# Optimization experiments

Measured on AMD Instinct MI355X. Metric: run time of the kernel, lower is better.

Reference implementation:

```python
import jax, jax.numpy as jnp
import numpy as np

B, S, T, D = 8, 8, 256, 256          # batch, series, time_steps, input_dim
H, DK = 8, 64                         # attn_heads, attn_dim
HD = H * DK                           # 512
L = 2                                 # attn_layers
F = 256                               # mlp_dim
R = 512                               # resolution
M = 128                               # number of mid-points sampled this step
EPS = 1e-5


def setup_inputs() -> dict:
    key = jax.random.key(0)
    ks = iter(jax.random.split(key, 64))

    def rn(shape, scale=0.05):
        return scale * jax.random.normal(next(ks), shape, dtype=jnp.float32)

    inp = {
        'encoded': jax.random.normal(next(ks), (B, S, T, D), dtype=jnp.float32),
        'true_u': jax.random.uniform(next(ks), (B, S, T), dtype=jnp.float32),
        'mid_idx': jnp.sort(jax.random.randint(next(ks), (M,), 0, T)),
        'left_idx': jax.random.randint(next(ks), (M,), 0, T),
        'right_idx': jax.random.randint(next(ks), (M,), 0, T),
        'i': 3,
        # dimension_shift
        'ds_W': rn((D, HD)), 'ds_b': jnp.zeros((HD,), jnp.float32),
        # per-layer, per-head key-creator MLPs (stacked): (D+1) -> F -> F -> DK
        'kW1': rn((L, H, D + 1, F)), 'kb1': jnp.zeros((L, H, F), jnp.float32),
        'kW2': rn((L, H, F, F)),     'kb2': jnp.zeros((L, H, F), jnp.float32),
        'kW3': rn((L, H, F, DK)),    'kb3': jnp.zeros((L, H, DK), jnp.float32),
        # value-creator MLPs
        'vW1': rn((L, H, D + 1, F)), 'vb1': jnp.zeros((L, H, F), jnp.float32),
        'vW2': rn((L, H, F, F)),     'vb2': jnp.zeros((L, H, F), jnp.float32),
        'vW3': rn((L, H, F, DK)),    'vb3': jnp.zeros((L, H, DK), jnp.float32),
        # attention / feed-forward layer norms
        'ln1_g': jnp.ones((L, HD), jnp.float32), 'ln1_b': jnp.zeros((L, HD), jnp.float32),
        'ln2_g': jnp.ones((L, HD), jnp.float32), 'ln2_b': jnp.zeros((L, HD), jnp.float32),
        # feed-forwards
        'ffW1': rn((L, HD, HD)), 'ffb1': jnp.zeros((L, HD), jnp.float32),
        'ffW2': rn((L, HD, HD)), 'ffb2': jnp.zeros((L, HD), jnp.float32),
        # dist_extractors MLP: HD -> F -> F -> R
        'deW1': rn((HD, F)), 'deb1': jnp.zeros((F,), jnp.float32),
        'deW2': rn((F, F)),  'deb2': jnp.zeros((F,), jnp.float32),
        'deW3': rn((F, R)),  'deb3': jnp.zeros((R,), jnp.float32),
    }
    return inp


def _mlp_heads(x, W1, b1, W2, b2, W3, b3):
    # x: [B,S,T,D+1]; weights: [L,H,...] -> out [L,B,S,T,H,DK]
    h = jax.nn.relu(jnp.einsum('bstc,lhcf->lbsthf', x, W1) + b1[:, None, None, None])
    h = jax.nn.relu(jnp.einsum('lbsthf,lhfg->lbsthg', h, W2) + b2[:, None, None, None])
    return jnp.einsum('lbsthg,lhgd->lbsthd', h, W3) + b3[:, None, None, None]


def _ln(x, g, b):
    mu = jnp.mean(x, axis=-1, keepdims=True)
    var = jnp.mean(jnp.square(x - mu), axis=-1, keepdims=True)
    return (x - mu) * jax.lax.rsqrt(var + EPS) * g + b


def reference(encoded, true_u, mid_idx, left_idx, right_idx, i,
              ds_W, ds_b,
              kW1, kb1, kW2, kb2, kW3, kb3,
              vW1, vb1, vW2, vb2, vW3, vb3,
              ln1_g, ln1_b, ln2_g, ln2_b,
              ffW1, ffb1, ffW2, ffb2,
              deW1, deb1, deW2, deb2, deW3, deb3):
    # merged_input = cat([encoded, true_u[..., None]])  -> [B,S,T,D+1]
    merged = jnp.concatenate([encoded, true_u[..., None]], axis=-1)

    keys = _mlp_heads(merged, kW1, kb1, kW2, kb2, kW3, kb3)   # [L,B,S,T,H,DK]
    values = _mlp_heads(merged, vW1, vb1, vW2, vb2, vW3, vb3)  # [L,B,S,T,H,DK]

    srange = jnp.arange(S)
    # n=1 neighbor: time index = loop counter m for series < i, else right[m]
    # (faithful to keys_hist[:, :i, mid:mid+1] in the original)
    idx1 = jnp.where(srange[None, :] < i, jnp.arange(M)[:, None], right_idx[:, None])  # [M,S]

    def gather_neighbors(kv):  # kv: [L,B,S,T,H,DK] -> [L,B,M,S,2,H,DK]
        n0 = jnp.transpose(kv[:, :, :, left_idx], (0, 1, 3, 2, 4, 5))  # [L,B,M,S,H,DK]
        n1 = kv[:, :, srange[None, :], idx1]                            # [L,B,M,S,H,DK]
        return jnp.stack([n0, n1], axis=4)

    nk = gather_neighbors(keys)
    nv = gather_neighbors(values)

    pred = encoded[:, i, mid_idx]                  # [B,M,D]
    att_value = pred @ ds_W + ds_b                 # [B,M,HD]

    scale = DK ** (-0.5)
    for l in range(L):
        avh = att_value.reshape(B, M, H, DK)
        prod = jnp.einsum('bmhd,bmsnhd->bmhsn', avh, nk[l]) * scale
        w = jax.nn.softmax(prod, axis=-1)          # softmax over n only, as in source
        att = jnp.einsum('bmhsn,bmsnhd->bmhd', w, nv[l]).reshape(B, M, HD)
        x = _ln(att_value + att, ln1_g[l], ln1_b[l])
        ff = jax.nn.relu(x @ ffW1[l] + ffb1[l]) @ ffW2[l] + ffb2[l]
        att_value = _ln(x + ff, ln2_g[l], ln2_b[l])

    h = jax.nn.relu(att_value @ deW1 + deb1)
    h = jax.nn.relu(h @ deW2 + deb2)
    logits = h @ deW3 + deb3                       # [B,M,R]
    return logits
```

## Files before the change

kernel.cpp:

```cpp
#include <hip/hip_runtime.h>
#include <hip/hip_bf16.h>

#define NB 8
#define NS 8
#define NT 256
#define ND 256
#define NH 8
#define NDK 64
#define NHD 512
#define NL 2
#define NF 256
#define NR 512
#define NM 128
#define NTOK 16384
#define NROW 1024

typedef __attribute__((ext_vector_type(8))) short short8;
typedef __attribute__((ext_vector_type(4))) float f32x4;

__device__ __forceinline__ unsigned short f2bf(float x) {
    unsigned u = __builtin_bit_cast(unsigned, x);
    unsigned r = (u + 0x7fffu + ((u >> 16) & 1u)) >> 16;
    return (unsigned short)r;
}
__device__ __forceinline__ float bf2f(unsigned short x) {
    return __builtin_bit_cast(float, ((unsigned)x) << 16);
}
__device__ __forceinline__ float wred(float v) {
#pragma unroll
    for (int o = 32; o > 0; o >>= 1) v += __shfl_xor(v, o, 64);
    return v;
}

__global__ __launch_bounds__(256) void prep_all(
    const float* __restrict__ enc,
    const float* __restrict__ kW1, const float* __restrict__ kW2, const float* __restrict__ kW3,
    const float* __restrict__ vW1, const float* __restrict__ vW2, const float* __restrict__ vW3,
    const float* __restrict__ dsW, const float* __restrict__ ffW1,
    const float* __restrict__ ffW2, const float* __restrict__ deW1,
    const float* __restrict__ deW2, const float* __restrict__ deW3,
    unsigned short* __restrict__ XF, unsigned short* __restrict__ WP,
    float* __restrict__ W1L, unsigned short* __restrict__ WG) {
    __shared__ float T[32][257];
    int bid = blockIdx.x, tid = threadIdx.x;
    if (bid < 512) {
        int t0 = bid * 32;
        const float* src = enc + (size_t)t0 * 256;
#pragma unroll
        for (int it = 0; it < 8; ++it) {
            int f4 = it * 256 + tid;
            int row = f4 >> 6, c = (f4 & 63) * 4;
            float4 v = *(const float4*)(src + row * 256 + c);
            T[row][c] = v.x; T[row][c + 1] = v.y; T[row][c + 2] = v.z; T[row][c + 3] = v.w;
        }
        __syncthreads();
        int tile = t0 >> 7, g = (t0 >> 6) & 1, nt0 = (t0 >> 4) & 3;
#pragma unroll
        for (int i = 0; i < 32; i += 8) {
            int o = tid * 32 + i;
            int lane = (o >> 3) & 63, ntp = (o >> 9) & 1, kc = o >> 10;
            int id = lane & 15, quad = lane >> 4;
            __align__(16) unsigned short p[8];
#pragma unroll
            for (int j = 0; j < 8; ++j) p[j] = f2bf(T[ntp * 16 + id][kc * 32 + quad * 8 + j]);
            size_t dsto = ((size_t)((((tile * 8 + kc) * 2 + g) * 4 + (nt0 + ntp)) * 64 + lane)) * 8;
            *(uint4*)(XF + dsto) = *(uint4*)p;
        }
    } else if (bid < 1280) {
        int lb = bid - 512;
        int combo = lb / 24, r = lb % 24;
        int st = r >> 3, kc = r & 7;
        int kvv = combo >> 4, l = (combo >> 3) & 1, h = combo & 7;
        unsigned short* dstc = WP + (size_t)combo * 147456;
        if (st < 2) {
            const float* W = (st == 0) ? (kvv ? vW1 : kW1) : (kvv ? vW2 : kW2);
            int rows = (st == 0) ? 257 : 256;
            const float* src = W + ((size_t)(l * 8 + h) * rows + kc * 32) * 256;
#pragma unroll
            for (int it = 0; it < 8; ++it) {
                int f4 = it * 256 + tid;
                int row = f4 >> 6, c = (f4 & 63) * 4;
                float4 v = *(const float4*)(src + (size_t)row * 256 + c);
                T[row][c] = v.x; T[row][c + 1] = v.y; T[row][c + 2] = v.z; T[row][c + 3] = v.w;
            }
            __syncthreads();
            unsigned short* dst = dstc + st * 65536 + kc * 8192;
#pragma unroll
            for (int i = 0; i < 32; i += 8) {
                int o = tid * 32 + i;
                int lane = (o >> 3) & 63, ftile = o >> 9;
                int id = lane & 15, quad = lane >> 4;
                __align__(16) unsigned short p[8];
#pragma unroll
                for (int j = 0; j < 8; ++j) p[j] = f2bf(T[quad * 8 + j][ftile * 16 + id]);
                *(uint4*)(dst + o) = *(uint4*)p;
            }
            if (st == 0 && kc == 0) {
                const float* hw = (kvv ? vW1 : kW1) + (size_t)(l * 8 + h) * 257 * 256;
                W1L[combo * 256 + tid] = hw[65536 + tid];
            }
        } else {
            const float* src = (kvv ? vW3 : kW3) + ((size_t)(l * 8 + h) * 256 + kc * 32) * 64;
#pragma unroll
            for (int it = 0; it < 2; ++it) {
                int f4 = it * 256 + tid;
                int row = f4 >> 4, c = (f4 & 15) * 4;
                float4 v = *(const float4*)(src + (size_t)row * 64 + c);
                T[row][c] = v.x; T[row][c + 1] = v.y; T[row][c + 2] = v.z; T[row][c + 3] = v.w;
            }
            __syncthreads();
            unsigned short* dst = dstc + 131072 + kc * 2048;
            int o = tid * 8;
            int lane = tid & 63, ftile = tid >> 6;
            int id = lane & 15, quad = lane >> 4;
            __align__(16) unsigned short p[8];
#pragma unroll
            for (int j = 0; j < 8; ++j) p[j] = f2bf(T[quad * 8 + j][ftile * 16 + id]);
            *(uint4*)(dst + o) = *(uint4*)p;
        }
    } else {
        int lb0 = bid - 1280;
        const float* src; int N, kc, ng; size_t base;
        if (lb0 < 32)       { int lb = lb0;       src = dsW;           N = 512; base = 0;       kc = lb >> 2; ng = lb & 3; }
        else if (lb0 < 96)  { int lb = lb0 - 32;  src = ffW1;          N = 512; base = 131072;  kc = lb >> 2; ng = lb & 3; }
        else if (lb0 < 160) { int lb = lb0 - 96;  src = ffW1 + 262144; N = 512; base = 393216;  kc = lb >> 2; ng = lb & 3; }
        else if (lb0 < 224) { int lb = lb0 - 160; src = ffW2;          N = 512; base = 655360;  kc = lb >> 2; ng = lb & 3; }
        else if (lb0 < 288) { int lb = lb0 - 224; src = ffW2 + 262144; N = 512; base = 917504;  kc = lb >> 2; ng = lb & 3; }
        else if (lb0 < 320) { int lb = lb0 - 288; src = deW1;          N = 256; base = 1179648; kc = lb >> 1; ng = lb & 1; }
        else if (lb0 < 336) { int lb = lb0 - 320; src = deW2;          N = 256; base = 1310720; kc = lb >> 1; ng = lb & 1; }
        else                { int lb = lb0 - 336; src = deW3;          N = 512; base = 1376256; kc = lb >> 2; ng = lb & 3; }
        int NTl = N >> 4;
        const float* s = src + (size_t)(kc * 32) * N + ng * 128;
#pragma unroll
        for (int it = 0; it < 4; ++it) {
            int f4 = it * 256 + tid;
            int row = f4 >> 5, c = (f4 & 31) * 4;
            float4 v = *(const float4*)(s + (size_t)row * N + c);
            T[row][c] = v.x; T[row][c + 1] = v.y; T[row][c + 2] = v.z; T[row][c + 3] = v.w;
        }
        __syncthreads();
        unsigned short* d = WG + base + (size_t)(kc * NTl + ng * 8) * 512;
#pragma unroll
        for (int i = 0; i < 16; i += 8) {
            int o = tid * 16 + i;
            int lane = (o >> 3) & 63, ntl = o >> 9;
            int id = lane & 15, quad = lane >> 4;
            __align__(16) unsigned short p[8];
#pragma unroll
            for (int j = 0; j < 8; ++j) p[j] = f2bf(T[quad * 8 + j][ntl * 16 + id]);
            *(uint4*)(d + o) = *(uint4*)p;
        }
    }
}

__global__ __launch_bounds__(256, 4) void heads_mlp(
    const float* __restrict__ tu, const unsigned short* __restrict__ XF,
    const unsigned short* __restrict__ WP, const float* __restrict__ W1L,
    const float* __restrict__ kb1, const float* __restrict__ kb2, const float* __restrict__ kb3,
    const float* __restrict__ vb1, const float* __restrict__ vb2, const float* __restrict__ vb3,
    unsigned short* __restrict__ KV) {
    __shared__ __align__(16) unsigned short smem[16896];

    const int tid = threadIdx.x;
    const int w2 = tid >> 6, lane = tid & 63, id = lane & 15, quad = lane >> 4;
    const int combo = blockIdx.x & 31, t64 = blockIdx.x >> 5;
    const int kvv = combo >> 4, l = (combo >> 3) & 1, h = combo & 7;
    const int r0 = t64 * 64;
    const int tile128 = t64 >> 1, g = t64 & 1;
    const unsigned short* WF1 = WP + (size_t)combo * 147456;
    const unsigned short* WF2 = WF1 + 65536;
    const unsigned short* WF3 = WF1 + 131072;
    const float* b1 = (kvv ? vb1 : kb1) + (l * 8 + h) * 256;
    const float* b2 = (kvv ? vb2 : kb2) + (l * 8 + h) * 256;
    const float* b3 = (kvv ? vb3 : kb3) + (l * 8 + h) * 64;

    {
        const uint4* s = (const uint4*)(XF + (size_t)tile128 * 32768 + g * 2048);
        uint4* d = (uint4*)smem;
#pragma unroll
        for (int kc = 0; kc < 8; ++kc) d[kc * 256 + tid] = s[kc * 512 + tid];
    }
    __syncthreads();

    f32x4 acc[4][4];
#pragma unroll
    for (int i = 0; i < 4; ++i)
#pragma unroll
        for (int j = 0; j < 4; ++j) acc[i][j] = (f32x4){0.f, 0.f, 0.f, 0.f};

    {
        short8 af[4], afn[4];
#pragma unroll
        for (int ft = 0; ft < 4; ++ft)
            af[ft] = *(const short8*)(WF1 + (size_t)((w2 * 4 + ft) * 64 + lane) * 8);
#pragma unroll
        for (int kc = 0; kc < 8; ++kc) {
            if (kc < 7) {
#pragma unroll
                for (int ft = 0; ft < 4; ++ft)
                    afn[ft] = *(const short8*)(WF1 + (size_t)(((kc + 1) * 16 + w2 * 4 + ft) * 64 + lane) * 8);
            }
            short8 bf[4];
#pragma unroll
            for (int nt = 0; nt < 4; ++nt)
                bf[nt] = *(const short8*)(smem + (size_t)(kc * 4 + nt) * 512 + lane * 8);
#pragma unroll
            for (int ft = 0; ft < 4; ++ft)
#pragma unroll
                for (int nt = 0; nt < 4; ++nt)
                    acc[ft][nt] = __builtin_amdgcn_mfma_f32_16x16x32_bf16(af[ft], bf[nt], acc[ft][nt], 0, 0, 0);
#pragma unroll
            for (int ft = 0; ft < 4; ++ft) af[ft] = afn[ft];
        }
    }
    __syncthreads();
    {
        float ur[4];
#pragma unroll
        for (int nt = 0; nt < 4; ++nt) ur[nt] = tu[r0 + nt * 16 + id];
#pragma unroll
        for (int ft = 0; ft < 4; ++ft) {
            int fb = w2 * 64 + ft * 16 + quad * 4;
            float4 bb = *(const float4*)(b1 + fb);
            float4 wl = *(const float4*)(W1L + combo * 256 + fb);
            const float* bbp = (const float*)&bb;
            const float* wlp = (const float*)&wl;
#pragma unroll
            for (int nt = 0; nt < 4; ++nt) {
                unsigned short p[4];
#pragma unroll
                for (int r = 0; r < 4; ++r) {
                    float v = acc[ft][nt][r] + bbp[r] + ur[nt] * wlp[r];
                    p[r] = f2bf(fmaxf(v, 0.f));
                }
                uint2 pk;
                pk.x = (unsigned)p[0] | ((unsigned)p[1] << 16);
                pk.y = (unsigned)p[2] | ((unsigned)p[3] << 16);
                *(uint2*)(smem + (size_t)(nt * 16 + id) * 264 + fb) = pk;
            }
        }
    }
    __syncthreads();

#pragma unroll
    for (int i = 0; i < 4; ++i)
#pragma unroll
        for (int j = 0; j < 4; ++j) acc[i][j] = (f32x4){0.f, 0.f, 0.f, 0.f};
    {
        short8 af[4], afn[4];
#pragma unroll
        for (int ft = 0; ft < 4; ++ft)
            af[ft] = *(const short8*)(WF2 + (size_t)((w2 * 4 + ft) * 64 + lane) * 8);
#pragma unroll
        for (int kc = 0; kc < 8; ++kc) {
            if (kc < 7) {
#pragma unroll
                for (int ft = 0; ft < 4; ++ft)
                    afn[ft] = *(const short8*)(WF2 + (size_t)(((kc + 1) * 16 + w2 * 4 + ft) * 64 + lane) * 8);
            }
            short8 bf[4];
#pragma unroll
            for (int nt = 0; nt < 4; ++nt)
                bf[nt] = *(const short8*)(smem + (size_t)(nt * 16 + id) * 264 + kc * 32 + quad * 8);
#pragma unroll
            for (int ft = 0; ft < 4; ++ft)
#pragma unroll
                for (int nt = 0; nt < 4; ++nt)
                    acc[ft][nt] = __builtin_amdgcn_mfma_f32_16x16x32_bf16(af[ft], bf[nt], acc[ft][nt], 0, 0, 0);
#pragma unroll
            for (int ft = 0; ft < 4; ++ft) af[ft] = afn[ft];
        }
    }
    __syncthreads();
#pragma unroll
    for (int ft = 0; ft < 4; ++ft) {
        int fb = w2 * 64 + ft * 16 + quad * 4;
        float4 bb = *(const float4*)(b2 + fb);
        const float* bbp = (const float*)&bb;
#pragma unroll
        for (int nt = 0; nt < 4; ++nt) {
            unsigned short p[4];
#pragma unroll
            for (int r = 0; r < 4; ++r)
                p[r] = f2bf(fmaxf(acc[ft][nt][r] + bbp[r], 0.f));
            uint2 pk;
            pk.x = (unsigned)p[0] | ((unsigned)p[1] << 16);
            pk.y = (unsigned)p[2] | ((unsigned)p[3] << 16);
            *(uint2*)(smem + (size_t)(nt * 16 + id) * 264 + fb) = pk;
        }
    }
    __syncthreads();

    f32x4 a3[4];
#pragma unroll
    for (int i = 0; i < 4; ++i) a3[i] = (f32x4){0.f, 0.f, 0.f, 0.f};
    {
        short8 af3[4], af3n[4];
#pragma unroll
        for (int ft = 0; ft < 4; ++ft)
            af3[ft] = *(const short8*)(WF3 + (size_t)(ft * 64 + lane) * 8);
#pragma unroll
        for (int kc = 0; kc < 8; ++kc) {
            if (kc < 7) {
#pragma unroll
                for (int ft = 0; ft < 4; ++ft)
                    af3n[ft] = *(const short8*)(WF3 + (size_t)(((kc + 1) * 4 + ft) * 64 + lane) * 8);
            }
            short8 b3f = *(const short8*)(smem + (size_t)(w2 * 16 + id) * 264 + kc * 32 + quad * 8);
#pragma unroll
            for (int ft = 0; ft < 4; ++ft)
                a3[ft] = __builtin_amdgcn_mfma_f32_16x16x32_bf16(af3[ft], b3f, a3[ft], 0, 0, 0);
#pragma unroll
            for (int ft = 0; ft < 4; ++ft) af3[ft] = af3n[ft];
        }
    }
    __syncthreads();
    {
        int tl = w2 * 16 + id;
#pragma unroll
        for (int ft = 0; ft < 4; ++ft) {
            int dk0 = ft * 16 + quad * 4;
            float4 bb = *(const float4*)(b3 + dk0);
            const float* bbp = (const float*)&bb;
            unsigned short p[4];
#pragma unroll
            for (int r = 0; r < 4; ++r) p[r] = f2bf(a3[ft][r] + bbp[r]);
            uint2 pk;
            pk.x = (unsigned)p[0] | ((unsigned)p[1] << 16);
            pk.y = (unsigned)p[2] | ((unsigned)p[3] << 16);
            *(uint2*)(smem + (size_t)tl * 72 + dk0) = pk;
        }
    }
    __syncthreads();
    {
#pragma unroll
        for (int it = 0; it < 2; ++it) {
            int tl = it * 32 + (tid >> 3), part = tid & 7;
            uint4 v = *(const uint4*)(smem + (size_t)tl * 72 + part * 8);
            size_t base = ((size_t)((l * 2 + kvv) * NTOK + r0 + tl)) * 512 + h * 64 + part * 8;
            *(uint4*)(KV + base) = v;
        }
    }
}

__global__ __launch_bounds__(256) void gemm_ds(
    const float* __restrict__ enc, const int* __restrict__ mid,
    const int* __restrict__ ip, const unsigned short* __restrict__ WF,
    const float* __restrict__ bias, float* __restrict__ outf) {
    int tid = threadIdx.x, wv = tid >> 6, lane = tid & 63;
    int id = lane & 15, quad = lane >> 4;
    int ntile = blockIdx.x * 4 + wv;
    int n0 = ntile * 16, m0 = blockIdx.y * 32;
    int iv = ip[0];
    int r0 = m0 + id, r1 = m0 + 16 + id;
    const float* a0p = enc + (((size_t)((r0 >> 7) * 8 + iv)) * 256 + mid[r0 & 127]) * 256 + quad * 8;
    const float* a1p = enc + (((size_t)((r1 >> 7) * 8 + iv)) * 256 + mid[r1 & 127]) * 256 + quad * 8;
    f32x4 acc[2];
    acc[0] = (f32x4){0.f, 0.f, 0.f, 0.f};
    acc[1] = (f32x4){0.f, 0.f, 0.f, 0.f};
#pragma unroll
    for (int kc = 0; kc < 8; ++kc) {
        short8 bw = *(const short8*)(WF + (size_t)((kc * 32 + ntile) * 64 + lane) * 8);
        float4 u0 = *(const float4*)(a0p + kc * 32);
        float4 u1 = *(const float4*)(a0p + kc * 32 + 4);
        float4 w0 = *(const float4*)(a1p + kc * 32);
        float4 w1 = *(const float4*)(a1p + kc * 32 + 4);
        short8 a0, a1;
        a0[0] = (short)f2bf(u0.x); a0[1] = (short)f2bf(u0.y); a0[2] = (short)f2bf(u0.z); a0[3] = (short)f2bf(u0.w);
        a0[4] = (short)f2bf(u1.x); a0[5] = (short)f2bf(u1.y); a0[6] = (short)f2bf(u1.z); a0[7] = (short)f2bf(u1.w);
        a1[0] = (short)f2bf(w0.x); a1[1] = (short)f2bf(w0.y); a1[2] = (short)f2bf(w0.z); a1[3] = (short)f2bf(w0.w);
        a1[4] = (short)f2bf(w1.x); a1[5] = (short)f2bf(w1.y); a1[6] = (short)f2bf(w1.z); a1[7] = (short)f2bf(w1.w);
        acc[0] = __builtin_amdgcn_mfma_f32_16x16x32_bf16(a0, bw, acc[0], 0, 0, 0);
        acc[1] = __builtin_amdgcn_mfma_f32_16x16x32_bf16(a1, bw, acc[1], 0, 0, 0);
    }
    float bv = bias[n0 + id];
#pragma unroll
    for (int mt = 0; mt < 2; ++mt) {
#pragma unroll
        for (int r = 0; r < 4; ++r) {
            int row = m0 + mt * 16 + quad * 4 + r;
            outf[(size_t)row * 512 + n0 + id] = acc[mt][r] + bv;
        }
    }
}

__global__ __launch_bounds__(256) void gemm_bf16(
    const unsigned short* __restrict__ A, const unsigned short* __restrict__ WF,
    const float* __restrict__ bias, const float* __restrict__ res,
    float* __restrict__ outf, unsigned short* __restrict__ outb,
    int K, int N, int relu) {
    int tid = threadIdx.x, wv = tid >> 6, lane = tid & 63;
    int id = lane & 15, quad = lane >> 4;
    int ntile = blockIdx.x * 4 + wv;
    int n0 = ntile * 16, m0 = blockIdx.y * 32;
    int NTl = N >> 4, KC = K >> 5;
    f32x4 acc[2];
    acc[0] = (f32x4){0.f, 0.f, 0.f, 0.f};
    acc[1] = (f32x4){0.f, 0.f, 0.f, 0.f};
    short8 bw = *(const short8*)(WF + (size_t)(ntile * 64 + lane) * 8);
    short8 a0 = *(const short8*)(A + (size_t)(m0 + id) * K + quad * 8);
    short8 a1 = *(const short8*)(A + (size_t)(m0 + 16 + id) * K + quad * 8);
    for (int kc = 0; kc < KC; ++kc) {
        short8 bwn, a0n, a1n;
        if (kc + 1 < KC) {
            bwn = *(const short8*)(WF + (size_t)(((kc + 1) * NTl + ntile) * 64 + lane) * 8);
            a0n = *(const short8*)(A + (size_t)(m0 + id) * K + (kc + 1) * 32 + quad * 8);
            a1n = *(const short8*)(A + (size_t)(m0 + 16 + id) * K + (kc + 1) * 32 + quad * 8);
        }
        acc[0] = __builtin_amdgcn_mfma_f32_16x16x32_bf16(a0, bw, acc[0], 0, 0, 0);
        acc[1] = __builtin_amdgcn_mfma_f32_16x16x32_bf16(a1, bw, acc[1], 0, 0, 0);
        bw = bwn; a0 = a0n; a1 = a1n;
    }
    float bv = bias[n0 + id];
#pragma unroll
    for (int mt = 0; mt < 2; ++mt) {
#pragma unroll
        for (int r = 0; r < 4; ++r) {
            int row = m0 + mt * 16 + quad * 4 + r;
            int n = n0 + id;
            float v = acc[mt][r] + bv;
            if (res) v += res[(size_t)row * N + n];
            if (relu) v = fmaxf(v, 0.f);
            if (outf) outf[(size_t)row * N + n] = v;
            if (outb) outb[(size_t)row * N + n] = f2bf(v);
        }
    }
}

__global__ __launch_bounds__(256) void attn_ln(
    const float* __restrict__ attv, const unsigned short* __restrict__ keys,
    const unsigned short* __restrict__ vals, const int* __restrict__ left,
    const int* __restrict__ right, const int* __restrict__ ip,
    const float* __restrict__ g, const float* __restrict__ bb,
    float* __restrict__ xout, unsigned short* __restrict__ xoutb) {
    int tid = threadIdx.x, wv = tid >> 6, lane = tid & 63;
    int gid = blockIdx.x * 4 + wv;
    int b = gid >> 7, m = gid & 127;
    int iv = ip[0];
    int lt = left[m], rt = right[m];
    float av8[8], att8[8];
    {
        const float* avp = attv + (size_t)gid * 512 + lane * 8;
        float4 u0 = *(const float4*)(avp);
        float4 u1 = *(const float4*)(avp + 4);
        av8[0] = u0.x; av8[1] = u0.y; av8[2] = u0.z; av8[3] = u0.w;
        av8[4] = u1.x; av8[5] = u1.y; av8[6] = u1.z; av8[7] = u1.w;
    }
#pragma unroll
    for (int j = 0; j < 8; ++j) att8[j] = 0.f;
    for (int s = 0; s < 8; ++s) {
        int t1 = (s < iv) ? m : rt;
        size_t row0 = ((size_t)((b * 8 + s) * 256 + lt)) * 512 + lane * 8;
        size_t row1 = ((size_t)((b * 8 + s) * 256 + t1)) * 512 + lane * 8;
        uint4 k0u = *(const uint4*)(keys + row0);
        uint4 k1u = *(const uint4*)(keys + row1);
        uint4 v0u = *(const uint4*)(vals + row0);
        uint4 v1u = *(const uint4*)(vals + row1);
        const unsigned short* k0 = (const unsigned short*)&k0u;
        const unsigned short* k1 = (const unsigned short*)&k1u;
        const unsigned short* v0 = (const unsigned short*)&v0u;
        const unsigned short* v1 = (const unsigned short*)&v1u;
        float p0 = 0.f, p1 = 0.f;
#pragma unroll
        for (int j = 0; j < 8; ++j) {
            p0 += av8[j] * bf2f(k0[j]);
            p1 += av8[j] * bf2f(k1[j]);
        }
#pragma unroll
        for (int o = 1; o < 8; o <<= 1) {
            p0 += __shfl_xor(p0, o, 64);
            p1 += __shfl_xor(p1, o, 64);
        }
        p0 *= 0.125f; p1 *= 0.125f;
        float mx = fmaxf(p0, p1);
        float e0 = __expf(p0 - mx), e1 = __expf(p1 - mx);
        float inv = 1.f / (e0 + e1);
        float w0 = e0 * inv, w1 = e1 * inv;
#pragma unroll
        for (int j = 0; j < 8; ++j)
            att8[j] += w0 * bf2f(v0[j]) + w1 * bf2f(v1[j]);
    }
    float x8[8], sum = 0.f;
#pragma unroll
    for (int j = 0; j < 8; ++j) { x8[j] = av8[j] + att8[j]; sum += x8[j]; }
    float mu = wred(sum) * (1.f / 512.f);
    float s2 = 0.f;
#pragma unroll
    for (int j = 0; j < 8; ++j) { float d = x8[j] - mu; s2 += d * d; }
    float rs = rsqrtf(wred(s2) * (1.f / 512.f) + 1e-5f);
    {
        const float* gp = g + lane * 8;
        const float* bp = bb + lane * 8;
        float* of = xout + (size_t)gid * 512 + lane * 8;
        unsigned short* ob = xoutb + (size_t)gid * 512 + lane * 8;
        __align__(16) float vout[8];
        __align__(16) unsigned short pb[8];
#pragma unroll
        for (int j = 0; j < 8; ++j) {
            float v = (x8[j] - mu) * rs * gp[j] + bp[j];
            vout[j] = v; pb[j] = f2bf(v);
        }
        *(float4*)(of) = *(float4*)vout;
        *(float4*)(of + 4) = *(float4*)(vout + 4);
        *(uint4*)(ob) = *(uint4*)pb;
    }
}

__global__ __launch_bounds__(256) void ln_k(const float* __restrict__ in,
                                            const float* __restrict__ g,
                                            const float* __restrict__ bb,
                                            float* __restrict__ out,
                                            unsigned short* __restrict__ outb) {
    int tid = threadIdx.x, wv = tid >> 6, lane = tid & 63;
    int gid = blockIdx.x * 4 + wv;
    float x8[8], sum = 0.f;
    {
        const float* ip = in + (size_t)gid * 512 + lane * 8;
        float4 u0 = *(const float4*)(ip);
        float4 u1 = *(const float4*)(ip + 4);
        x8[0] = u0.x; x8[1] = u0.y; x8[2] = u0.z; x8[3] = u0.w;
        x8[4] = u1.x; x8[5] = u1.y; x8[6] = u1.z; x8[7] = u1.w;
    }
#pragma unroll
    for (int j = 0; j < 8; ++j) sum += x8[j];
    float mu = wred(sum) * (1.f / 512.f);
    float s2 = 0.f;
#pragma unroll
    for (int j = 0; j < 8; ++j) { float d = x8[j] - mu; s2 += d * d; }
    float rs = rsqrtf(wred(s2) * (1.f / 512.f) + 1e-5f);
    {
        const float* gp = g + lane * 8;
        const float* bp = bb + lane * 8;
        float* of = out + (size_t)gid * 512 + lane * 8;
        unsigned short* ob = outb + (size_t)gid * 512 + lane * 8;
        __align__(16) float vout[8];
        __align__(16) unsigned short pb[8];
#pragma unroll
        for (int j = 0; j < 8; ++j) {
            float v = (x8[j] - mu) * rs * gp[j] + bp[j];
            vout[j] = v; pb[j] = f2bf(v);
        }
        *(float4*)(of) = *(float4*)vout;
        *(float4*)(of + 4) = *(float4*)(vout + 4);
        *(uint4*)(ob) = *(uint4*)pb;
    }
}

extern "C" void kernel_launch(void* const* d_in, const int* in_sizes, int n_in,
                              void* d_out, int out_size, void* d_ws, size_t ws_size,
                              hipStream_t stream) {
    const float* encoded = (const float*)d_in[0];
    const float* true_u  = (const float*)d_in[1];
    const int* mid_idx   = (const int*)d_in[2];
    const int* left_idx  = (const int*)d_in[3];
    const int* right_idx = (const int*)d_in[4];
    const int* ip        = (const int*)d_in[5];
    const float* ds_W = (const float*)d_in[6];
    const float* ds_b = (const float*)d_in[7];
    const float* kW1 = (const float*)d_in[8];
    const float* kb1 = (const float*)d_in[9];
    const float* kW2 = (const float*)d_in[10];
    const float* kb2 = (const float*)d_in[11];
    const float* kW3 = (const float*)d_in[12];
    const float* kb3 = (const float*)d_in[13];
    const float* vW1 = (const float*)d_in[14];
    const float* vb1 = (const float*)d_in[15];
    const float* vW2 = (const float*)d_in[16];
    const float* vb2 = (const float*)d_in[17];
    const float* vW3 = (const float*)d_in[18];
    const float* vb3 = (const float*)d_in[19];
    const float* ln1_g = (const float*)d_in[20];
    const float* ln1_b = (const float*)d_in[21];
    const float* ln2_g = (const float*)d_in[22];
    const float* ln2_b = (const float*)d_in[23];
    const float* ffW1 = (const float*)d_in[24];
    const float* ffb1 = (const float*)d_in[25];
    const float* ffW2 = (const float*)d_in[26];
    const float* ffb2 = (const float*)d_in[27];
    const float* deW1 = (const float*)d_in[28];
    const float* deb1 = (const float*)d_in[29];
    const float* deW2 = (const float*)d_in[30];
    const float* deb2 = (const float*)d_in[31];
    const float* deW3 = (const float*)d_in[32];
    const float* deb3 = (const float*)d_in[33];

    char* ws = (char*)d_ws;
    unsigned short* XF   = (unsigned short*)(ws + 0);
    unsigned short* WP   = (unsigned short*)(ws + 8388608);
    float* W1L           = (float*)(ws + 17825792);
    unsigned short* KV   = (unsigned short*)(ws + 17858560);
    unsigned short* WG   = (unsigned short*)(ws + 84967424);
    float* ATTV          = (float*)(ws + 87982080);
    float* XBUF          = (float*)(ws + 90079232);
    float* YBUF          = (float*)(ws + 92176384);
    unsigned short* ATTVB = (unsigned short*)(ws + 94797824);
    unsigned short* XBUFB = (unsigned short*)(ws + 95846400);
    unsigned short* FBUFB = (unsigned short*)(ws + 96894976);
    unsigned short* DE1B = XBUFB;
    unsigned short* DE2B = FBUFB;

    unsigned short* WGds  = WG + 0;
    unsigned short* WGff1_0 = WG + 131072;
    unsigned short* WGff1_1 = WG + 393216;
    unsigned short* WGff2_0 = WG + 655360;
    unsigned short* WGff2_1 = WG + 917504;
    unsigned short* WGde1 = WG + 1179648;
    unsigned short* WGde2 = WG + 1310720;
    unsigned short* WGde3 = WG + 1376256;

    prep_all<<<1648, 256, 0, stream>>>(encoded, kW1, kW2, kW3, vW1, vW2, vW3,
                                       ds_W, ffW1, ffW2, deW1, deW2, deW3,
                                       XF, WP, W1L, WG);
    heads_mlp<<<8192, 256, 0, stream>>>(true_u, XF, WP, W1L, kb1, kb2, kb3,
                                        vb1, vb2, vb3, KV);
    gemm_ds<<<dim3(8, 32), 256, 0, stream>>>(encoded, mid_idx, ip, WGds, ds_b, ATTV);
    for (int l = 0; l < 2; ++l) {
        const unsigned short* keys = KV + (size_t)(l * 2) * NTOK * NHD;
        const unsigned short* vals = KV + (size_t)(l * 2 + 1) * NTOK * NHD;
        attn_ln<<<256, 256, 0, stream>>>(ATTV, keys, vals, left_idx, right_idx, ip,
                                         ln1_g + l * 512, ln1_b + l * 512, XBUF, XBUFB);
        gemm_bf16<<<dim3(8, 32), 256, 0, stream>>>(XBUFB, (l ? WGff1_1 : WGff1_0),
                                                   ffb1 + l * 512, nullptr,
                                                   nullptr, FBUFB, 512, 512, 1);
        gemm_bf16<<<dim3(8, 32), 256, 0, stream>>>(FBUFB, (l ? WGff2_1 : WGff2_0),
                                                   ffb2 + l * 512, XBUF,
                                                   YBUF, nullptr, 512, 512, 0);
        ln_k<<<256, 256, 0, stream>>>(YBUF, ln2_g + l * 512, ln2_b + l * 512, ATTV, ATTVB);
    }
    gemm_bf16<<<dim3(4, 32), 256, 0, stream>>>(ATTVB, WGde1, deb1, nullptr,
                                               nullptr, DE1B, 512, 256, 1);
    gemm_bf16<<<dim3(4, 32), 256, 0, stream>>>(DE1B, WGde2, deb2, nullptr,
                                               nullptr, DE2B, 256, 256, 1);
    gemm_bf16<<<dim3(8, 32), 256, 0, stream>>>(DE2B, WGde3, deb3, nullptr,
                                               (float*)d_out, nullptr, 256, 512, 0);
}
```

Measured before the change: 431.0 us.

## Fuse attention, feed-forward, layer norms and decoder MLP into one tail kernel

```diff
diff --git a/kernel.cpp b/kernel.cpp
--- a/kernel.cpp
+++ b/kernel.cpp
@@ -163,7 +163,7 @@
 
     const int tid = threadIdx.x;
     const int w2 = tid >> 6, lane = tid & 63, id = lane & 15, quad = lane >> 4;
-    const int combo = blockIdx.x & 31, t64 = blockIdx.x >> 5;
+    const int combo = blockIdx.x >> 8, t64 = blockIdx.x & 255;
     const int kvv = combo >> 4, l = (combo >> 3) & 1, h = combo & 7;
     const int r0 = t64 * 64;
     const int tile128 = t64 >> 1, g = t64 & 1;
@@ -337,212 +337,328 @@
         for (int it = 0; it < 2; ++it) {
             int tl = it * 32 + (tid >> 3), part = tid & 7;
             uint4 v = *(const uint4*)(smem + (size_t)tl * 72 + part * 8);
-            size_t base = ((size_t)((l * 2 + kvv) * NTOK + r0 + tl)) * 512 + h * 64 + part * 8;
+            size_t base = ((size_t)combo << 20) + (size_t)(r0 + tl) * 64 + part * 8;
             *(uint4*)(KV + base) = v;
         }
     }
 }
 
-__global__ __launch_bounds__(256) void gemm_ds(
+__global__ __launch_bounds__(256) void fused_tail(
     const float* __restrict__ enc, const int* __restrict__ mid,
-    const int* __restrict__ ip, const unsigned short* __restrict__ WF,
-    const float* __restrict__ bias, float* __restrict__ outf) {
-    int tid = threadIdx.x, wv = tid >> 6, lane = tid & 63;
-    int id = lane & 15, quad = lane >> 4;
-    int ntile = blockIdx.x * 4 + wv;
-    int n0 = ntile * 16, m0 = blockIdx.y * 32;
-    int iv = ip[0];
-    int r0 = m0 + id, r1 = m0 + 16 + id;
-    const float* a0p = enc + (((size_t)((r0 >> 7) * 8 + iv)) * 256 + mid[r0 & 127]) * 256 + quad * 8;
-    const float* a1p = enc + (((size_t)((r1 >> 7) * 8 + iv)) * 256 + mid[r1 & 127]) * 256 + quad * 8;
-    f32x4 acc[2];
-    acc[0] = (f32x4){0.f, 0.f, 0.f, 0.f};
-    acc[1] = (f32x4){0.f, 0.f, 0.f, 0.f};
-#pragma unroll
-    for (int kc = 0; kc < 8; ++kc) {
-        short8 bw = *(const short8*)(WF + (size_t)((kc * 32 + ntile) * 64 + lane) * 8);
-        float4 u0 = *(const float4*)(a0p + kc * 32);
-        float4 u1 = *(const float4*)(a0p + kc * 32 + 4);
-        float4 w0 = *(const float4*)(a1p + kc * 32);
-        float4 w1 = *(const float4*)(a1p + kc * 32 + 4);
-        short8 a0, a1;
-        a0[0] = (short)f2bf(u0.x); a0[1] = (short)f2bf(u0.y); a0[2] = (short)f2bf(u0.z); a0[3] = (short)f2bf(u0.w);
-        a0[4] = (short)f2bf(u1.x); a0[5] = (short)f2bf(u1.y); a0[6] = (short)f2bf(u1.z); a0[7] = (short)f2bf(u1.w);
-        a1[0] = (short)f2bf(w0.x); a1[1] = (short)f2bf(w0.y); a1[2] = (short)f2bf(w0.z); a1[3] = (short)f2bf(w0.w);
-        a1[4] = (short)f2bf(w1.x); a1[5] = (short)f2bf(w1.y); a1[6] = (short)f2bf(w1.z); a1[7] = (short)f2bf(w1.w);
-        acc[0] = __builtin_amdgcn_mfma_f32_16x16x32_bf16(a0, bw, acc[0], 0, 0, 0);
-        acc[1] = __builtin_amdgcn_mfma_f32_16x16x32_bf16(a1, bw, acc[1], 0, 0, 0);
-    }
-    float bv = bias[n0 + id];
-#pragma unroll
-    for (int mt = 0; mt < 2; ++mt) {
-#pragma unroll
-        for (int r = 0; r < 4; ++r) {
-            int row = m0 + mt * 16 + quad * 4 + r;
-            outf[(size_t)row * 512 + n0 + id] = acc[mt][r] + bv;
-        }
-    }
-}
-
-__global__ __launch_bounds__(256) void gemm_bf16(
-    const unsigned short* __restrict__ A, const unsigned short* __restrict__ WF,
-    const float* __restrict__ bias, const float* __restrict__ res,
-    float* __restrict__ outf, unsigned short* __restrict__ outb,
-    int K, int N, int relu) {
-    int tid = threadIdx.x, wv = tid >> 6, lane = tid & 63;
-    int id = lane & 15, quad = lane >> 4;
-    int ntile = blockIdx.x * 4 + wv;
-    int n0 = ntile * 16, m0 = blockIdx.y * 32;
-    int NTl = N >> 4, KC = K >> 5;
-    f32x4 acc[2];
-    acc[0] = (f32x4){0.f, 0.f, 0.f, 0.f};
-    acc[1] = (f32x4){0.f, 0.f, 0.f, 0.f};
-    short8 bw = *(const short8*)(WF + (size_t)(ntile * 64 + lane) * 8);
-    short8 a0 = *(const short8*)(A + (size_t)(m0 + id) * K + quad * 8);
-    short8 a1 = *(const short8*)(A + (size_t)(m0 + 16 + id) * K + quad * 8);
-    for (int kc = 0; kc < KC; ++kc) {
-        short8 bwn, a0n, a1n;
-        if (kc + 1 < KC) {
-            bwn = *(const short8*)(WF + (size_t)(((kc + 1) * NTl + ntile) * 64 + lane) * 8);
-            a0n = *(const short8*)(A + (size_t)(m0 + id) * K + (kc + 1) * 32 + quad * 8);
-            a1n = *(const short8*)(A + (size_t)(m0 + 16 + id) * K + (kc + 1) * 32 + quad * 8);
-        }
-        acc[0] = __builtin_amdgcn_mfma_f32_16x16x32_bf16(a0, bw, acc[0], 0, 0, 0);
-        acc[1] = __builtin_amdgcn_mfma_f32_16x16x32_bf16(a1, bw, acc[1], 0, 0, 0);
-        bw = bwn; a0 = a0n; a1 = a1n;
-    }
-    float bv = bias[n0 + id];
-#pragma unroll
-    for (int mt = 0; mt < 2; ++mt) {
-#pragma unroll
-        for (int r = 0; r < 4; ++r) {
-            int row = m0 + mt * 16 + quad * 4 + r;
-            int n = n0 + id;
-            float v = acc[mt][r] + bv;
-            if (res) v += res[(size_t)row * N + n];
-            if (relu) v = fmaxf(v, 0.f);
-            if (outf) outf[(size_t)row * N + n] = v;
-            if (outb) outb[(size_t)row * N + n] = f2bf(v);
-        }
-    }
-}
-
-__global__ __launch_bounds__(256) void attn_ln(
-    const float* __restrict__ attv, const unsigned short* __restrict__ keys,
-    const unsigned short* __restrict__ vals, const int* __restrict__ left,
-    const int* __restrict__ right, const int* __restrict__ ip,
-    const float* __restrict__ g, const float* __restrict__ bb,
-    float* __restrict__ xout, unsigned short* __restrict__ xoutb) {
-    int tid = threadIdx.x, wv = tid >> 6, lane = tid & 63;
-    int gid = blockIdx.x * 4 + wv;
-    int b = gid >> 7, m = gid & 127;
-    int iv = ip[0];
-    int lt = left[m], rt = right[m];
-    float av8[8], att8[8];
-    {
-        const float* avp = attv + (size_t)gid * 512 + lane * 8;
-        float4 u0 = *(const float4*)(avp);
-        float4 u1 = *(const float4*)(avp + 4);
-        av8[0] = u0.x; av8[1] = u0.y; av8[2] = u0.z; av8[3] = u0.w;
-        av8[4] = u1.x; av8[5] = u1.y; av8[6] = u1.z; av8[7] = u1.w;
-    }
-#pragma unroll
-    for (int j = 0; j < 8; ++j) att8[j] = 0.f;
-    for (int s = 0; s < 8; ++s) {
-        int t1 = (s < iv) ? m : rt;
-        size_t row0 = ((size_t)((b * 8 + s) * 256 + lt)) * 512 + lane * 8;
-        size_t row1 = ((size_t)((b * 8 + s) * 256 + t1)) * 512 + lane * 8;
-        uint4 k0u = *(const uint4*)(keys + row0);
-        uint4 k1u = *(const uint4*)(keys + row1);
-        uint4 v0u = *(const uint4*)(vals + row0);
-        uint4 v1u = *(const uint4*)(vals + row1);
-        const unsigned short* k0 = (const unsigned short*)&k0u;
-        const unsigned short* k1 = (const unsigned short*)&k1u;
-        const unsigned short* v0 = (const unsigned short*)&v0u;
-        const unsigned short* v1 = (const unsigned short*)&v1u;
-        float p0 = 0.f, p1 = 0.f;
-#pragma unroll
-        for (int j = 0; j < 8; ++j) {
-            p0 += av8[j] * bf2f(k0[j]);
-            p1 += av8[j] * bf2f(k1[j]);
-        }
-#pragma unroll
-        for (int o = 1; o < 8; o <<= 1) {
-            p0 += __shfl_xor(p0, o, 64);
-            p1 += __shfl_xor(p1, o, 64);
-        }
-        p0 *= 0.125f; p1 *= 0.125f;
-        float mx = fmaxf(p0, p1);
-        float e0 = __expf(p0 - mx), e1 = __expf(p1 - mx);
-        float inv = 1.f / (e0 + e1);
-        float w0 = e0 * inv, w1 = e1 * inv;
-#pragma unroll
-        for (int j = 0; j < 8; ++j)
-            att8[j] += w0 * bf2f(v0[j]) + w1 * bf2f(v1[j]);
-    }
-    float x8[8], sum = 0.f;
-#pragma unroll
-    for (int j = 0; j < 8; ++j) { x8[j] = av8[j] + att8[j]; sum += x8[j]; }
-    float mu = wred(sum) * (1.f / 512.f);
-    float s2 = 0.f;
-#pragma unroll
-    for (int j = 0; j < 8; ++j) { float d = x8[j] - mu; s2 += d * d; }
-    float rs = rsqrtf(wred(s2) * (1.f / 512.f) + 1e-5f);
-    {
-        const float* gp = g + lane * 8;
-        const float* bp = bb + lane * 8;
-        float* of = xout + (size_t)gid * 512 + lane * 8;
-        unsigned short* ob = xoutb + (size_t)gid * 512 + lane * 8;
-        __align__(16) float vout[8];
-        __align__(16) unsigned short pb[8];
-#pragma unroll
-        for (int j = 0; j < 8; ++j) {
-            float v = (x8[j] - mu) * rs * gp[j] + bp[j];
-            vout[j] = v; pb[j] = f2bf(v);
-        }
-        *(float4*)(of) = *(float4*)vout;
-        *(float4*)(of + 4) = *(float4*)(vout + 4);
-        *(uint4*)(ob) = *(uint4*)pb;
-    }
-}
-
-__global__ __launch_bounds__(256) void ln_k(const float* __restrict__ in,
-                                            const float* __restrict__ g,
-                                            const float* __restrict__ bb,
-                                            float* __restrict__ out,
-                                            unsigned short* __restrict__ outb) {
-    int tid = threadIdx.x, wv = tid >> 6, lane = tid & 63;
-    int gid = blockIdx.x * 4 + wv;
-    float x8[8], sum = 0.f;
-    {
-        const float* ip = in + (size_t)gid * 512 + lane * 8;
-        float4 u0 = *(const float4*)(ip);
-        float4 u1 = *(const float4*)(ip + 4);
-        x8[0] = u0.x; x8[1] = u0.y; x8[2] = u0.z; x8[3] = u0.w;
-        x8[4] = u1.x; x8[5] = u1.y; x8[6] = u1.z; x8[7] = u1.w;
-    }
-#pragma unroll
-    for (int j = 0; j < 8; ++j) sum += x8[j];
-    float mu = wred(sum) * (1.f / 512.f);
-    float s2 = 0.f;
-#pragma unroll
-    for (int j = 0; j < 8; ++j) { float d = x8[j] - mu; s2 += d * d; }
-    float rs = rsqrtf(wred(s2) * (1.f / 512.f) + 1e-5f);
-    {
-        const float* gp = g + lane * 8;
-        const float* bp = bb + lane * 8;
-        float* of = out + (size_t)gid * 512 + lane * 8;
-        unsigned short* ob = outb + (size_t)gid * 512 + lane * 8;
-        __align__(16) float vout[8];
-        __align__(16) unsigned short pb[8];
-#pragma unroll
-        for (int j = 0; j < 8; ++j) {
-            float v = (x8[j] - mu) * rs * gp[j] + bp[j];
-            vout[j] = v; pb[j] = f2bf(v);
-        }
-        *(float4*)(of) = *(float4*)vout;
-        *(float4*)(of + 4) = *(float4*)(vout + 4);
-        *(uint4*)(ob) = *(uint4*)pb;
+    const int* __restrict__ left, const int* __restrict__ right,
+    const int* __restrict__ ip,
+    const unsigned short* __restrict__ KV, const unsigned short* __restrict__ WG,
+    const float* __restrict__ ds_b,
+    const float* __restrict__ ln1_g, const float* __restrict__ ln1_b,
+    const float* __restrict__ ln2_g, const float* __restrict__ ln2_b,
+    const float* __restrict__ ffb1, const float* __restrict__ ffb2,
+    const float* __restrict__ deb1, const float* __restrict__ deb2,
+    const float* __restrict__ deb3, float* __restrict__ out) {
+    extern __shared__ __align__(16) char fsm[];
+    float* sXF = (float*)fsm;
+    float* sYF = (float*)(fsm + 33280);
+    unsigned short* sXB = (unsigned short*)(fsm + 66560);
+    unsigned short* sHB = (unsigned short*)(fsm + 82944);
+
+    const int tid = threadIdx.x;
+    const int w = tid >> 6, lane = tid & 63, id = lane & 15, quad = lane >> 4;
+    const int r0 = blockIdx.x * 16;
+    const int iv = ip[0];
+
+    {
+        int grow = r0 + id;
+        int bI = grow >> 7, mI = grow & 127;
+        const float* ap = enc + (((size_t)(bI * 8 + iv)) * 256 + mid[mI]) * 256 + quad * 8;
+        f32x4 acc[8];
+#pragma unroll
+        for (int i = 0; i < 8; ++i) acc[i] = (f32x4){0.f, 0.f, 0.f, 0.f};
+#pragma unroll
+        for (int kc = 0; kc < 8; ++kc) {
+            float4 u0 = *(const float4*)(ap + kc * 32);
+            float4 u1 = *(const float4*)(ap + kc * 32 + 4);
+            short8 a;
+            a[0] = (short)f2bf(u0.x); a[1] = (short)f2bf(u0.y); a[2] = (short)f2bf(u0.z); a[3] = (short)f2bf(u0.w);
+            a[4] = (short)f2bf(u1.x); a[5] = (short)f2bf(u1.y); a[6] = (short)f2bf(u1.z); a[7] = (short)f2bf(u1.w);
+#pragma unroll
+            for (int ntj = 0; ntj < 8; ++ntj) {
+                short8 bw = *(const short8*)(WG + (size_t)((kc * 32 + w * 8 + ntj) * 64 + lane) * 8);
+                acc[ntj] = __builtin_amdgcn_mfma_f32_16x16x32_bf16(a, bw, acc[ntj], 0, 0, 0);
+            }
+        }
+#pragma unroll
+        for (int ntj = 0; ntj < 8; ++ntj) {
+            int n = ((w * 8 + ntj) << 4) + id;
+            float bv = ds_b[n];
+#pragma unroll
+            for (int r = 0; r < 4; ++r) {
+                int row = quad * 4 + r;
+                float v = acc[ntj][r] + bv;
+                sXF[row * 520 + n] = v;
+                sXB[((n >> 5) << 9) + (((n >> 3) & 3) << 7) + (row << 3) + (n & 7)] = f2bf(v);
+            }
+        }
+    }
+    __syncthreads();
+
+    for (int l = 0; l < 2; ++l) {
+        {
+            int h = lane >> 3, d8 = lane & 7;
+            const unsigned short* kb = KV + ((size_t)(l * 8 + h) << 20);
+            const unsigned short* vb = KV + ((size_t)(16 + l * 8 + h) << 20);
+            const float* g1 = ln1_g + l * 512;
+            const float* bb1 = ln1_b + l * 512;
+            for (int rr = 0; rr < 4; ++rr) {
+                int row = w * 4 + rr;
+                int gid = r0 + row;
+                int bI = gid >> 7, mI = gid & 127;
+                int lt = left[mI], rt = right[mI];
+                float av8[8], att8[8];
+                {
+                    float4 u0 = *(const float4*)(sXF + row * 520 + lane * 8);
+                    float4 u1 = *(const float4*)(sXF + row * 520 + lane * 8 + 4);
+                    av8[0] = u0.x; av8[1] = u0.y; av8[2] = u0.z; av8[3] = u0.w;
+                    av8[4] = u1.x; av8[5] = u1.y; av8[6] = u1.z; av8[7] = u1.w;
+                }
+#pragma unroll
+                for (int j = 0; j < 8; ++j) att8[j] = 0.f;
+#pragma unroll
+                for (int s = 0; s < 8; ++s) {
+                    int t1 = (s < iv) ? mI : rt;
+                    size_t o0 = (size_t)((bI * 8 + s) * 256 + lt) * 64 + d8 * 8;
+                    size_t o1 = (size_t)((bI * 8 + s) * 256 + t1) * 64 + d8 * 8;
+                    uint4 k0u = *(const uint4*)(kb + o0);
+                    uint4 k1u = *(const uint4*)(kb + o1);
+                    uint4 v0u = *(const uint4*)(vb + o0);
+                    uint4 v1u = *(const uint4*)(vb + o1);
+                    const unsigned short* k0 = (const unsigned short*)&k0u;
+                    const unsigned short* k1 = (const unsigned short*)&k1u;
+                    const unsigned short* v0 = (const unsigned short*)&v0u;
+                    const unsigned short* v1 = (const unsigned short*)&v1u;
+                    float p0 = 0.f, p1 = 0.f;
+#pragma unroll
+                    for (int j = 0; j < 8; ++j) {
+                        p0 += av8[j] * bf2f(k0[j]);
+                        p1 += av8[j] * bf2f(k1[j]);
+                    }
+#pragma unroll
+                    for (int o = 1; o < 8; o <<= 1) {
+                        p0 += __shfl_xor(p0, o, 64);
+                        p1 += __shfl_xor(p1, o, 64);
+                    }
+                    p0 *= 0.125f; p1 *= 0.125f;
+                    float mx = fmaxf(p0, p1);
+                    float e0 = __expf(p0 - mx), e1 = __expf(p1 - mx);
+                    float inv = 1.f / (e0 + e1);
+                    float w0 = e0 * inv, w1 = e1 * inv;
+#pragma unroll
+                    for (int j = 0; j < 8; ++j)
+                        att8[j] += w0 * bf2f(v0[j]) + w1 * bf2f(v1[j]);
+                }
+                float x8[8], sum = 0.f;
+#pragma unroll
+                for (int j = 0; j < 8; ++j) { x8[j] = av8[j] + att8[j]; sum += x8[j]; }
+                float mu = wred(sum) * (1.f / 512.f);
+                float s2 = 0.f;
+#pragma unroll
+                for (int j = 0; j < 8; ++j) { float d = x8[j] - mu; s2 += d * d; }
+                float rs = rsqrtf(wred(s2) * (1.f / 512.f) + 1e-5f);
+                float4 g0 = *(const float4*)(g1 + lane * 8);
+                float4 g4 = *(const float4*)(g1 + lane * 8 + 4);
+                float4 bb0 = *(const float4*)(bb1 + lane * 8);
+                float4 bb4 = *(const float4*)(bb1 + lane * 8 + 4);
+                const float* gp = (const float*)&g0;
+                __align__(16) float gv[8], bv[8], vout[8];
+                *(float4*)gv = g0; *(float4*)(gv + 4) = g4;
+                *(float4*)bv = bb0; *(float4*)(bv + 4) = bb4;
+                __align__(16) unsigned short pb[8];
+#pragma unroll
+                for (int j = 0; j < 8; ++j) {
+                    float v = (x8[j] - mu) * rs * gv[j] + bv[j];
+                    vout[j] = v; pb[j] = f2bf(v);
+                }
+                (void)gp;
+                *(float4*)(sXF + row * 520 + lane * 8) = *(float4*)vout;
+                *(float4*)(sXF + row * 520 + lane * 8 + 4) = *(float4*)(vout + 4);
+                *(uint4*)(sXB + ((lane >> 2) << 9) + ((lane & 3) << 7) + (row << 3)) = *(uint4*)pb;
+            }
+        }
+        __syncthreads();
+        {
+            const unsigned short* Wf = WG + 131072 + (size_t)l * 262144;
+            const float* bia = ffb1 + l * 512;
+            f32x4 acc[8];
+#pragma unroll
+            for (int i = 0; i < 8; ++i) acc[i] = (f32x4){0.f, 0.f, 0.f, 0.f};
+            for (int kc = 0; kc < 16; ++kc) {
+                short8 a = *(const short8*)(sXB + ((kc << 6) + lane) * 8);
+#pragma unroll
+                for (int ntj = 0; ntj < 8; ++ntj) {
+                    short8 bw = *(const short8*)(Wf + (size_t)((kc * 32 + w * 8 + ntj) * 64 + lane) * 8);
+                    acc[ntj] = __builtin_amdgcn_mfma_f32_16x16x32_bf16(a, bw, acc[ntj], 0, 0, 0);
+                }
+            }
+#pragma unroll
+            for (int ntj = 0; ntj < 8; ++ntj) {
+                int n = ((w * 8 + ntj) << 4) + id;
+                float bv = bia[n];
+#pragma unroll
+                for (int r = 0; r < 4; ++r) {
+                    int row = quad * 4 + r;
+                    float v = fmaxf(acc[ntj][r] + bv, 0.f);
+                    sHB[((n >> 5) << 9) + (((n >> 3) & 3) << 7) + (row << 3) + (n & 7)] = f2bf(v);
+                }
+            }
+        }
+        __syncthreads();
+        {
+            const unsigned short* Wf = WG + 655360 + (size_t)l * 262144;
+            const float* bia = ffb2 + l * 512;
+            f32x4 acc[8];
+#pragma unroll
+            for (int i = 0; i < 8; ++i) acc[i] = (f32x4){0.f, 0.f, 0.f, 0.f};
+            for (int kc = 0; kc < 16; ++kc) {
+                short8 a = *(const short8*)(sHB + ((kc << 6) + lane) * 8);
+#pragma unroll
+                for (int ntj = 0; ntj < 8; ++ntj) {
+                    short8 bw = *(const short8*)(Wf + (size_t)((kc * 32 + w * 8 + ntj) * 64 + lane) * 8);
+                    acc[ntj] = __builtin_amdgcn_mfma_f32_16x16x32_bf16(a, bw, acc[ntj], 0, 0, 0);
+                }
+            }
+#pragma unroll
+            for (int ntj = 0; ntj < 8; ++ntj) {
+                int n = ((w * 8 + ntj) << 4) + id;
+                float bv = bia[n];
+#pragma unroll
+                for (int r = 0; r < 4; ++r) {
+                    int row = quad * 4 + r;
+                    sYF[row * 520 + n] = acc[ntj][r] + bv + sXF[row * 520 + n];
+                }
+            }
+        }
+        __syncthreads();
+        {
+            const float* g2 = ln2_g + l * 512;
+            const float* bb2 = ln2_b + l * 512;
+            for (int rr = 0; rr < 4; ++rr) {
+                int row = w * 4 + rr;
+                float x8[8], sum = 0.f;
+                {
+                    float4 u0 = *(const float4*)(sYF + row * 520 + lane * 8);
+                    float4 u1 = *(const float4*)(sYF + row * 520 + lane * 8 + 4);
+                    x8[0] = u0.x; x8[1] = u0.y; x8[2] = u0.z; x8[3] = u0.w;
+                    x8[4] = u1.x; x8[5] = u1.y; x8[6] = u1.z; x8[7] = u1.w;
+                }
+#pragma unroll
+                for (int j = 0; j < 8; ++j) sum += x8[j];
+                float mu = wred(sum) * (1.f / 512.f);
+                float s2 = 0.f;
+#pragma unroll
+                for (int j = 0; j < 8; ++j) { float d = x8[j] - mu; s2 += d * d; }
+                float rs = rsqrtf(wred(s2) * (1.f / 512.f) + 1e-5f);
+                __align__(16) float gv[8], bv[8], vout[8];
+                *(float4*)gv = *(const float4*)(g2 + lane * 8);
+                *(float4*)(gv + 4) = *(const float4*)(g2 + lane * 8 + 4);
+                *(float4*)bv = *(const float4*)(bb2 + lane * 8);
+                *(float4*)(bv + 4) = *(const float4*)(bb2 + lane * 8 + 4);
+                __align__(16) unsigned short pb[8];
+#pragma unroll
+                for (int j = 0; j < 8; ++j) {
+                    float v = (x8[j] - mu) * rs * gv[j] + bv[j];
+                    vout[j] = v; pb[j] = f2bf(v);
+                }
+                *(float4*)(sXF + row * 520 + lane * 8) = *(float4*)vout;
+                *(float4*)(sXF + row * 520 + lane * 8 + 4) = *(float4*)(vout + 4);
+                *(uint4*)(sXB + ((lane >> 2) << 9) + ((lane & 3) << 7) + (row << 3)) = *(uint4*)pb;
+            }
+        }
+        __syncthreads();
+    }
+
+    {
+        const unsigned short* Wf = WG + 1179648;
+        f32x4 acc[4];
+#pragma unroll
+        for (int i = 0; i < 4; ++i) acc[i] = (f32x4){0.f, 0.f, 0.f, 0.f};
+        for (int kc = 0; kc < 16; ++kc) {
+            short8 a = *(const short8*)(sXB + ((kc << 6) + lane) * 8);
+#pragma unroll
+            for (int ntj = 0; ntj < 4; ++ntj) {
+                short8 bw = *(const short8*)(Wf + (size_t)((kc * 16 + w * 4 + ntj) * 64 + lane) * 8);
+                acc[ntj] = __builtin_amdgcn_mfma_f32_16x16x32_bf16(a, bw, acc[ntj], 0, 0, 0);
+            }
+        }
+#pragma unroll
+        for (int ntj = 0; ntj < 4; ++ntj) {
+            int n = ((w * 4 + ntj) << 4) + id;
+            float bv = deb1[n];
+#pragma unroll
+            for (int r = 0; r < 4; ++r) {
+                int row = quad * 4 + r;
+                float v = fmaxf(acc[ntj][r] + bv, 0.f);
+                sHB[((n >> 5) << 9) + (((n >> 3) & 3) << 7) + (row << 3) + (n & 7)] = f2bf(v);
+            }
+        }
+    }
+    __syncthreads();
+    {
+        const unsigned short* Wf = WG + 1310720;
+        f32x4 acc[4];
+#pragma unroll
+        for (int i = 0; i < 4; ++i) acc[i] = (f32x4){0.f, 0.f, 0.f, 0.f};
+        for (int kc = 0; kc < 8; ++kc) {
+            short8 a = *(const short8*)(sHB + ((kc << 6) + lane) * 8);
+#pragma unroll
+            for (int ntj = 0; ntj < 4; ++ntj) {
+                short8 bw = *(const short8*)(Wf + (size_t)((kc * 16 + w * 4 + ntj) * 64 + lane) * 8);
+                acc[ntj] = __builtin_amdgcn_mfma_f32_16x16x32_bf16(a, bw, acc[ntj], 0, 0, 0);
+            }
+        }
+#pragma unroll
+        for (int ntj = 0; ntj < 4; ++ntj) {
+            int n = ((w * 4 + ntj) << 4) + id;
+            float bv = deb2[n];
+#pragma unroll
+            for (int r = 0; r < 4; ++r) {
+                int row = quad * 4 + r;
+                float v = fmaxf(acc[ntj][r] + bv, 0.f);
+                sXB[((n >> 5) << 9) + (((n >> 3) & 3) << 7) + (row << 3) + (n & 7)] = f2bf(v);
+            }
+        }
+    }
+    __syncthreads();
+    {
+        const unsigned short* Wf = WG + 1376256;
+        f32x4 acc[8];
+#pragma unroll
+        for (int i = 0; i < 8; ++i) acc[i] = (f32x4){0.f, 0.f, 0.f, 0.f};
+        for (int kc = 0; kc < 8; ++kc) {
+            short8 a = *(const short8*)(sXB + ((kc << 6) + lane) * 8);
+#pragma unroll
+            for (int ntj = 0; ntj < 8; ++ntj) {
+                short8 bw = *(const short8*)(Wf + (size_t)((kc * 32 + w * 8 + ntj) * 64 + lane) * 8);
+                acc[ntj] = __builtin_amdgcn_mfma_f32_16x16x32_bf16(a, bw, acc[ntj], 0, 0, 0);
+            }
+        }
+#pragma unroll
+        for (int ntj = 0; ntj < 8; ++ntj) {
+            int n = ((w * 8 + ntj) << 4) + id;
+            float bv = deb3[n];
+#pragma unroll
+            for (int r = 0; r < 4; ++r) {
+                int row = quad * 4 + r;
+                sXF[row * 520 + n] = acc[ntj][r] + bv;
+            }
+        }
+    }
+    __syncthreads();
+    {
+#pragma unroll
+        for (int i = 0; i < 8; ++i) {
+            int idx = i * 256 + tid;
+            int row = idx >> 7, c4 = (idx & 127) * 4;
+            float4 v = *(const float4*)(sXF + row * 520 + c4);
+            *(float4*)(out + (size_t)(r0 + row) * 512 + c4) = v;
+        }
     }
 }
 
@@ -590,47 +706,14 @@
     float* W1L           = (float*)(ws + 17825792);
     unsigned short* KV   = (unsigned short*)(ws + 17858560);
     unsigned short* WG   = (unsigned short*)(ws + 84967424);
-    float* ATTV          = (float*)(ws + 87982080);
-    float* XBUF          = (float*)(ws + 90079232);
-    float* YBUF          = (float*)(ws + 92176384);
-    unsigned short* ATTVB = (unsigned short*)(ws + 94797824);
-    unsigned short* XBUFB = (unsigned short*)(ws + 95846400);
-    unsigned short* FBUFB = (unsigned short*)(ws + 96894976);
-    unsigned short* DE1B = XBUFB;
-    unsigned short* DE2B = FBUFB;
-
-    unsigned short* WGds  = WG + 0;
-    unsigned short* WGff1_0 = WG + 131072;
-    unsigned short* WGff1_1 = WG + 393216;
-    unsigned short* WGff2_0 = WG + 655360;
-    unsigned short* WGff2_1 = WG + 917504;
-    unsigned short* WGde1 = WG + 1179648;
-    unsigned short* WGde2 = WG + 1310720;
-    unsigned short* WGde3 = WG + 1376256;
 
     prep_all<<<1648, 256, 0, stream>>>(encoded, kW1, kW2, kW3, vW1, vW2, vW3,
                                        ds_W, ffW1, ffW2, deW1, deW2, deW3,
                                        XF, WP, W1L, WG);
     heads_mlp<<<8192, 256, 0, stream>>>(true_u, XF, WP, W1L, kb1, kb2, kb3,
                                         vb1, vb2, vb3, KV);
-    gemm_ds<<<dim3(8, 32), 256, 0, stream>>>(encoded, mid_idx, ip, WGds, ds_b, ATTV);
-    for (int l = 0; l < 2; ++l) {
-        const unsigned short* keys = KV + (size_t)(l * 2) * NTOK * NHD;
-        const unsigned short* vals = KV + (size_t)(l * 2 + 1) * NTOK * NHD;
-        attn_ln<<<256, 256, 0, stream>>>(ATTV, keys, vals, left_idx, right_idx, ip,
-                                         ln1_g + l * 512, ln1_b + l * 512, XBUF, XBUFB);
-        gemm_bf16<<<dim3(8, 32), 256, 0, stream>>>(XBUFB, (l ? WGff1_1 : WGff1_0),
-                                                   ffb1 + l * 512, nullptr,
-                                                   nullptr, FBUFB, 512, 512, 1);
-        gemm_bf16<<<dim3(8, 32), 256, 0, stream>>>(FBUFB, (l ? WGff2_1 : WGff2_0),
-                                                   ffb2 + l * 512, XBUF,
-                                                   YBUF, nullptr, 512, 512, 0);
-        ln_k<<<256, 256, 0, stream>>>(YBUF, ln2_g + l * 512, ln2_b + l * 512, ATTV, ATTVB);
-    }
-    gemm_bf16<<<dim3(4, 32), 256, 0, stream>>>(ATTVB, WGde1, deb1, nullptr,
-                                               nullptr, DE1B, 512, 256, 1);
-    gemm_bf16<<<dim3(4, 32), 256, 0, stream>>>(DE1B, WGde2, deb2, nullptr,
-                                               nullptr, DE2B, 256, 256, 1);
-    gemm_bf16<<<dim3(8, 32), 256, 0, stream>>>(DE2B, WGde3, deb3, nullptr,
-                                               (float*)d_out, nullptr, 256, 512, 0);
+    fused_tail<<<64, 256, 99328, stream>>>(encoded, mid_idx, left_idx, right_idx, ip,
+                                           KV, WG, ds_b, ln1_g, ln1_b, ln2_g, ln2_b,
+                                           ffb1, ffb2, deb1, deb2, deb3,
+                                           (float*)d_out);
 }
```

Result: slower. 587.0 us (+36.2%).
